# Kernel optimization log

Measured on AMD Instinct MI355X. Metric: run time of the kernel, lower is better.

The kernel has to match this reference:

```python
import jax, jax.numpy as jnp
import numpy as np

USER_NUM = 500000
ITEM_NUM = 100000
D = 256        # embedding_size
MEM = 32       # memory_size
ATT = 256      # attention_size
B = 4096       # batch
NF = 64        # friends per user (padded with index == USER_NUM)


def _u(k, shape):
    return jax.random.uniform(k, shape, dtype=jnp.float32, minval=-0.1, maxval=0.1)


def setup_inputs() -> dict:
    key = jax.random.key(0)
    ks = jax.random.split(key, 12)
    return {
        "input_u": jax.random.randint(ks[0], (B,), 0, USER_NUM + 1),
        "input_i": jax.random.randint(ks[1], (B,), 0, ITEM_NUM),
        "input_uf": jax.random.randint(ks[2], (B, NF), 0, USER_NUM + 1),
        "uidW": _u(ks[3], (USER_NUM + 1, D)),
        "iidW": _u(ks[4], (ITEM_NUM, D)),
        "i_bias": jnp.zeros((ITEM_NUM,), jnp.float32),
        "Key": _u(ks[5], (D, MEM)),
        "Mem": jnp.ones((MEM, D), jnp.float32),
        "WA": _u(ks[6], (D, ATT)),
        "BA": jnp.zeros((ATT,), jnp.float32),
        "U_omega": _u(ks[7], (ATT, 1)),
        "att_exp1": jax.random.normal(ks[8], (2 * D, 2), jnp.float32) * 0.05,
    }


def _l2norm(x, axis):
    # torch F.normalize(p=2): x / max(||x||, eps)
    n = jnp.sqrt(jnp.sum(x * x, axis=axis, keepdims=True))
    return x / jnp.maximum(n, 1e-12)


def reference(input_u, input_i, input_uf, uidW, iidW, i_bias, Key, Mem, WA, BA, U_omega, att_exp1):
    uid = uidW[input_u]                        # [B, D]
    iid = iidW[input_i]                        # [B, D]
    i_b = i_bias[input_i]                      # [B]
    fe = uidW[input_uf]                        # [B, F, D]
    frien_num = (input_uf != USER_NUM).astype(jnp.float32)  # [B, F] valid mask
    fe = frien_num[:, :, None] * fe

    uid_n = _l2norm(uid, axis=1)
    fe_n = _l2norm(fe, axis=2)
    cross = uid_n[:, None, :] * fe_n           # [B, F, D]

    att_key = jnp.einsum('bfd,dm->bfm', cross, Key)          # [B, F, M]
    att_mem = jax.nn.softmax(att_key, axis=0)                # NOTE: softmax over BATCH dim (faithful)
    att_mem = frien_num[:, :, None] * att_mem

    f1 = jnp.einsum('bfm,md->bfd', att_mem, Mem)             # [B, F, D]
    f2 = f1 * fe                                             # [B, F, D]

    h = jax.nn.relu(jnp.einsum('bfd,da->bfa', f2, WA) + BA)  # [B, F, A]
    j = jnp.exp(jnp.einsum('bfa,ao->bfo', h, U_omega))       # [B, F, 1]
    j = frien_num[:, :, None] * j
    w = j / (jnp.sum(j, axis=1, keepdims=True) + 1e-8)       # [B, F, 1]
    friend = jnp.sum(w * f2, axis=1)                         # [B, D]
    # dropout(p=dp) in eval mode -> identity

    user = uid + friend
    att1 = jax.nn.softmax(jnp.concatenate([uid, user], axis=1) @ att_exp1, axis=1)  # [B, 2]
    user_f = uid * att1[:, 0:1] + user * att1[:, 1:2]
    score = jnp.sum(user_f * iid, axis=1) + i_b              # [B]
    return score
```

## Files before the change

### kernel.cpp

```cpp
#include <hip/hip_runtime.h>

#define USER_NUM 500000
#define BATCH 4096
#define NF 64
#define DIM 256
#define MEMN 32
#define ATTN 256

typedef short bf16x8 __attribute__((ext_vector_type(8)));
typedef float f32x4 __attribute__((ext_vector_type(4)));

__device__ __forceinline__ unsigned short f2bf(float f) {
    unsigned u = __float_as_uint(f);
    u += 0x7FFFu + ((u >> 16) & 1u);
    return (unsigned short)(u >> 16);
}
__device__ __forceinline__ float bf2f(unsigned short s) {
    return __uint_as_float(((unsigned)s) << 16);
}
__device__ __forceinline__ bf16x8 as_frag(uint4 v) {
    return __builtin_bit_cast(bf16x8, v);
}

__device__ __forceinline__ float block_reduce_sum(float v, float* scr) {
#pragma unroll
    for (int o = 32; o; o >>= 1) v += __shfl_xor(v, o, 64);
    __syncthreads();
    if ((threadIdx.x & 63) == 0) scr[threadIdx.x >> 6] = v;
    __syncthreads();
    return scr[0] + scr[1] + scr[2] + scr[3];
}

#define WS_AK    0u
#define WS_FE    33554432u
#define WS_KEYT  167772160u
#define WS_MEMT  167788544u
#define WS_WATT  167804928u
#define WS_PART  167936000u
#define WS_SSUM  168001536u

__global__ __launch_bounds__(256) void kprep(const float* __restrict__ Key,
                                             const float* __restrict__ Mem,
                                             const float* __restrict__ WA,
                                             unsigned short* __restrict__ keyT,
                                             unsigned short* __restrict__ memT,
                                             unsigned short* __restrict__ watt) {
    int gid = blockIdx.x * 256 + threadIdx.x;
    if (gid < 8192) {
        int m = gid >> 8, d = gid & 255;
        keyT[gid] = f2bf(Key[d * 32 + m]);
    } else if (gid < 16384) {
        int e = gid - 8192, d = e >> 5, m = e & 31;
        memT[e] = f2bf(Mem[m * 256 + d]);
    } else {
        int e = gid - 16384;
        int kt = e >> 13, r = e & 8191, a = r >> 5, kk = r & 31;
        watt[e] = f2bf(WA[(kt * 32 + kk) * 256 + a]);
    }
}

__global__ __launch_bounds__(256, 4) void katt(const int* __restrict__ input_u,
                                               const int* __restrict__ input_uf,
                                               const float* __restrict__ uidW,
                                               const unsigned short* __restrict__ keyT_ws,
                                               unsigned short* __restrict__ fe_ws,
                                               float* __restrict__ ak) {
    extern __shared__ char smem[];
    float* uidn = (float*)(smem + 33792);
    float* scr  = (float*)(smem + 34816);
    int*   ufL  = (int*)(smem + 34880);
    float* mskL = (float*)(smem + 35136);
    const int b = blockIdx.x, t = threadIdx.x;
    const int w = t >> 6, l = t & 63, q = l >> 4;

    if (t < 64) {
        int uf = input_uf[b * NF + t];
        ufL[t] = uf;
        mskL[t] = (uf != USER_NUM) ? 1.0f : 0.0f;
    }
    int iu = input_u[b];
    float uv = uidW[(size_t)iu * DIM + t];
    float ss = block_reduce_sum(uv * uv, scr);
    float inv = 1.0f / fmaxf(sqrtf(ss), 1e-12f);
    uidn[t] = uv * inv;
    __syncthreads();

    float4 un4 = *(const float4*)(uidn + l * 4);
    float4 fe[16];
#pragma unroll
    for (int i = 0; i < 16; i++) {
        int idx = ufL[w * 16 + i];
        fe[i] = ((const float4*)(uidW + (size_t)idx * DIM))[l];
    }
#pragma unroll
    for (int i = 0; i < 16; i++) {
        int f = w * 16 + i;
        float mk = mskL[f];
        float x = fe[i].x * mk, y = fe[i].y * mk, z = fe[i].z * mk, ww = fe[i].w * mk;
        float s2 = x * x + y * y + z * z + ww * ww;
#pragma unroll
        for (int o = 32; o; o >>= 1) s2 += __shfl_xor(s2, o, 64);
        float rn = 1.0f / fmaxf(sqrtf(s2), 1e-12f);
        ushort4 fb;
        fb.x = f2bf(x); fb.y = f2bf(y); fb.z = f2bf(z); fb.w = f2bf(ww);
        *(ushort4*)(fe_ws + (size_t)b * 16384 + f * 256 + l * 4) = fb;
        ushort4 o4;
        o4.x = f2bf(un4.x * x * rn);
        o4.y = f2bf(un4.y * y * rn);
        o4.z = f2bf(un4.z * z * rn);
        o4.w = f2bf(un4.w * ww * rn);
        *(ushort4*)(smem + f * 528 + l * 8) = o4;
    }
    __syncthreads();

    const uint4* kp = (const uint4*)keyT_ws;
    f32x4 acc0 = {0.f, 0.f, 0.f, 0.f}, acc1 = {0.f, 0.f, 0.f, 0.f};
#pragma unroll
    for (int kt = 0; kt < 8; kt++) {
        bf16x8 aF = *(const bf16x8*)(smem + (w * 16 + (l & 15)) * 528 + kt * 64 + q * 16);
        bf16x8 b0 = as_frag(kp[(l & 15) * 32 + kt * 4 + q]);
        bf16x8 b1 = as_frag(kp[((l & 15) + 16) * 32 + kt * 4 + q]);
        acc0 = __builtin_amdgcn_mfma_f32_16x16x32_bf16(aF, b0, acc0, 0, 0, 0);
        acc1 = __builtin_amdgcn_mfma_f32_16x16x32_bf16(aF, b1, acc1, 0, 0, 0);
    }
    {
        int fbase = w * 16 + q * 4;
        int m = l & 15;
#pragma unroll
        for (int r = 0; r < 4; r++) {
            ak[((size_t)b * NF + fbase + r) * MEMN + m]      = acc0[r];
            ak[((size_t)b * NF + fbase + r) * MEMN + 16 + m] = acc1[r];
        }
    }
}

__global__ __launch_bounds__(256) void ksum1(const float* __restrict__ ak, float* __restrict__ part) {
    __shared__ float pl[256];
    int bid = blockIdx.x;
    int f = bid >> 3, c = bid & 7;
    int t = threadIdx.x, m = t & 31, g = t >> 5;
    float s = 0.f;
    size_t base = ((size_t)(c * 512 + g) * NF + f) * MEMN + m;
    for (int i = 0; i < 64; i++) {
        s += __expf(ak[base]);
        base += (size_t)8 * NF * MEMN;
    }
    pl[t] = s;
    __syncthreads();
    if (t < 32) {
        float tot = 0.f;
#pragma unroll
        for (int gg = 0; gg < 8; gg++) tot += pl[gg * 32 + t];
        part[c * 2048 + f * 32 + t] = tot;
    }
}
__global__ __launch_bounds__(256) void ksum2(const float* __restrict__ part, float* __restrict__ ssum) {
    int fm = blockIdx.x * 256 + threadIdx.x;
    float s = 0.f;
#pragma unroll
    for (int c = 0; c < 8; c++) s += part[c * 2048 + fm];
    ssum[fm] = s;
}

#define OFF_AM   33792
#define OFF_JP   38912
#define OFF_W    39936
#define OFF_MSK  40448
#define OFF_SCR  40704
__global__ __launch_bounds__(256, 3) void kmain(const int* __restrict__ input_u,
                                                const int* __restrict__ input_i,
                                                const int* __restrict__ input_uf,
                                                const float* __restrict__ uidW,
                                                const float* __restrict__ iidW,
                                                const float* __restrict__ i_bias,
                                                const float* __restrict__ BA,
                                                const float* __restrict__ U_omega,
                                                const float* __restrict__ att_exp1,
                                                const float* __restrict__ ak,
                                                const float* __restrict__ ssum_ws,
                                                const unsigned short* __restrict__ fe_ws,
                                                const unsigned short* __restrict__ memT_ws,
                                                const unsigned short* __restrict__ watt_ws,
                                                float* __restrict__ out) {
    extern __shared__ char smem[];
    float* jpL  = (float*)(smem + OFF_JP);
    float* wL   = (float*)(smem + OFF_W);
    float* mskL = (float*)(smem + OFF_MSK);
    float* scr  = (float*)(smem + OFF_SCR);
    const int b = blockIdx.x, t = threadIdx.x;
    const int w = t >> 6, l = t & 63, q = l >> 4;

    int iu = input_u[b], ii = input_i[b];
    float uidv = uidW[(size_t)iu * DIM + t];
    float iidv = iidW[(size_t)ii * DIM + t];
    float ib   = i_bias[ii];
    float ae00 = att_exp1[t * 2], ae01 = att_exp1[t * 2 + 1];
    float ae10 = att_exp1[(DIM + t) * 2], ae11 = att_exp1[(DIM + t) * 2 + 1];

    if (t < 64) {
        int uf = input_uf[b * NF + t];
        mskL[t] = (uf != USER_NUM) ? 1.0f : 0.0f;
    }
    __syncthreads();

    {
        const float4* akp = (const float4*)(ak + (size_t)b * 2048);
        const float4* sp  = (const float4*)ssum_ws;
        float4 a0 = akp[2 * t], a1 = akp[2 * t + 1];
        float4 s0 = sp[2 * t],  s1 = sp[2 * t + 1];
        float mk = mskL[t >> 2];
        float v0 = mk * __expf(a0.x) / s0.x;
        float v1 = mk * __expf(a0.y) / s0.y;
        float v2 = mk * __expf(a0.z) / s0.z;
        float v3 = mk * __expf(a0.w) / s0.w;
        float v4 = mk * __expf(a1.x) / s1.x;
        float v5 = mk * __expf(a1.y) / s1.y;
        float v6 = mk * __expf(a1.z) / s1.z;
        float v7 = mk * __expf(a1.w) / s1.w;
        uint4 pk;
        pk.x = (unsigned)f2bf(v0) | ((unsigned)f2bf(v1) << 16);
        pk.y = (unsigned)f2bf(v2) | ((unsigned)f2bf(v3) << 16);
        pk.z = (unsigned)f2bf(v4) | ((unsigned)f2bf(v5) << 16);
        pk.w = (unsigned)f2bf(v6) | ((unsigned)f2bf(v7) << 16);
        *(uint4*)(smem + OFF_AM + (t >> 2) * 80 + (t & 3) * 16) = pk;
    }
    __syncthreads();

    {
        const uint4* mp = (const uint4*)memT_ws;
        bf16x8 aF[4];
#pragma unroll
        for (int ft = 0; ft < 4; ft++)
            aF[ft] = *(const bf16x8*)(smem + OFF_AM + (ft * 16 + (l & 15)) * 80 + q * 16);
#pragma unroll
        for (int dti = 0; dti < 4; dti++) {
            int dt = 4 * w + dti;
            bf16x8 bF = as_frag(mp[(dt * 16 + (l & 15)) * 4 + q]);
            int dcol = dt * 16 + (l & 15);
#pragma unroll
            for (int ft = 0; ft < 4; ft++) {
                f32x4 acc = {0.f, 0.f, 0.f, 0.f};
                acc = __builtin_amdgcn_mfma_f32_16x16x32_bf16(aF[ft], bF, acc, 0, 0, 0);
                int fbase = ft * 16 + q * 4;
#pragma unroll
                for (int r = 0; r < 4; r++)
                    *(unsigned short*)(smem + (fbase + r) * 528 + dcol * 2) = f2bf(acc[r]);
            }
        }
    }
    __syncthreads();

    {
        ushort4 feb[16];
#pragma unroll
        for (int i = 0; i < 16; i++) {
            int f = w * 16 + i;
            feb[i] = *(const ushort4*)(fe_ws + (size_t)b * 16384 + f * 256 + l * 4);
        }
#pragma unroll
        for (int i = 0; i < 16; i++) {
            int f = w * 16 + i;
            ushort4* p = (ushort4*)(smem + f * 528 + l * 8);
            ushort4 fv = *p;
            ushort4 o4;
            o4.x = f2bf(bf2f(fv.x) * bf2f(feb[i].x));
            o4.y = f2bf(bf2f(fv.y) * bf2f(feb[i].y));
            o4.z = f2bf(bf2f(fv.z) * bf2f(feb[i].z));
            o4.w = f2bf(bf2f(fv.w) * bf2f(feb[i].w));
            *p = o4;
        }
    }
    __syncthreads();

    f32x4 acc[4][4];
    {
        f32x4 z = {0.f, 0.f, 0.f, 0.f};
#pragma unroll
        for (int ft = 0; ft < 4; ft++)
#pragma unroll
            for (int at = 0; at < 4; at++) acc[ft][at] = z;
    }
    {
        const uint4* wp = (const uint4*)watt_ws;
        for (int kt = 0; kt < 8; kt++) {
            bf16x8 aF[4], bF[4];
#pragma unroll
            for (int ft = 0; ft < 4; ft++)
                aF[ft] = *(const bf16x8*)(smem + (ft * 16 + (l & 15)) * 528 + kt * 64 + q * 16);
#pragma unroll
            for (int at = 0; at < 4; at++)
                bF[at] = as_frag(wp[kt * 1024 + (64 * w + at * 16 + (l & 15)) * 4 + q]);
#pragma unroll
            for (int ft = 0; ft < 4; ft++)
#pragma unroll
                for (int at = 0; at < 4; at++)
                    acc[ft][at] = __builtin_amdgcn_mfma_f32_16x16x32_bf16(aF[ft], bF[at], acc[ft][at], 0, 0, 0);
        }
    }
    {
        float jp[16];
#pragma unroll
        for (int i = 0; i < 16; i++) jp[i] = 0.f;
#pragma unroll
        for (int at = 0; at < 4; at++) {
            int a = 64 * w + at * 16 + (l & 15);
            float ba = BA[a], uw = U_omega[a];
#pragma unroll
            for (int ft = 0; ft < 4; ft++)
#pragma unroll
                for (int r = 0; r < 4; r++) {
                    float h = fmaxf(acc[ft][at][r] + ba, 0.f);
                    jp[ft * 4 + r] += h * uw;
                }
        }
#pragma unroll
        for (int mask = 1; mask < 16; mask <<= 1)
#pragma unroll
            for (int i = 0; i < 16; i++) jp[i] += __shfl_xor(jp[i], mask, 64);
        if ((l & 15) == 0) {
#pragma unroll
            for (int ft = 0; ft < 4; ft++)
#pragma unroll
                for (int r = 0; r < 4; r++)
                    jpL[w * 64 + ft * 16 + q * 4 + r] = jp[ft * 4 + r];
        }
    }
    __syncthreads();

    if (t < 64) {
        float logit = jpL[t] + jpL[64 + t] + jpL[128 + t] + jpL[192 + t];
        float jv = mskL[t] * __expf(logit);
        float s = jv;
#pragma unroll
        for (int o = 32; o; o >>= 1) s += __shfl_xor(s, o, 64);
        wL[t] = jv / (s + 1e-8f);
    }
    __syncthreads();

    float fr = 0.f;
#pragma unroll 8
    for (int f = 0; f < 64; f++)
        fr += wL[f] * bf2f(*(unsigned short*)(smem + f * 528 + t * 2));

    float user = uidv + fr;
    float l0 = block_reduce_sum(uidv * ae00 + user * ae10, scr);
    float l1 = block_reduce_sum(uidv * ae01 + user * ae11, scr);
    float mx = fmaxf(l0, l1);
    float e0 = __expf(l0 - mx), e1 = __expf(l1 - mx);
    float rinv = 1.0f / (e0 + e1);
    float a0w = e0 * rinv, a1w = e1 * rinv;
    float sc = block_reduce_sum((uidv * a0w + user * a1w) * iidv, scr);
    if (t == 0) out[b] = sc + ib;
}

extern "C" void kernel_launch(void* const* d_in, const int* in_sizes, int n_in,
                              void* d_out, int out_size, void* d_ws, size_t ws_size,
                              hipStream_t stream) {
    const int*   input_u  = (const int*)d_in[0];
    const int*   input_i  = (const int*)d_in[1];
    const int*   input_uf = (const int*)d_in[2];
    const float* uidW     = (const float*)d_in[3];
    const float* iidW     = (const float*)d_in[4];
    const float* i_bias   = (const float*)d_in[5];
    const float* Key      = (const float*)d_in[6];
    const float* Mem      = (const float*)d_in[7];
    const float* WA       = (const float*)d_in[8];
    const float* BA       = (const float*)d_in[9];
    const float* U_omega  = (const float*)d_in[10];
    const float* att_exp1 = (const float*)d_in[11];
    float* out = (float*)d_out;
    char* ws = (char*)d_ws;

    float*          ak   = (float*)(ws + WS_AK);
    unsigned short* fe   = (unsigned short*)(ws + WS_FE);
    unsigned short* keyT = (unsigned short*)(ws + WS_KEYT);
    unsigned short* memT = (unsigned short*)(ws + WS_MEMT);
    unsigned short* watt = (unsigned short*)(ws + WS_WATT);
    float*          part = (float*)(ws + WS_PART);
    float*          ssum = (float*)(ws + WS_SSUM);

    hipLaunchKernelGGL(kprep, dim3(320), dim3(256), 0, stream, Key, Mem, WA, keyT, memT, watt);
    hipLaunchKernelGGL(katt, dim3(BATCH), dim3(256), 35392, stream, input_u, input_uf, uidW, keyT, fe, ak);
    hipLaunchKernelGGL(ksum1, dim3(512), dim3(256), 0, stream, ak, part);
    hipLaunchKernelGGL(ksum2, dim3(8), dim3(256), 0, stream, part, ssum);
    hipLaunchKernelGGL(kmain, dim3(BATCH), dim3(256), 40768, stream, input_u, input_i, input_uf,
                       uidW, iidW, i_bias, BA, U_omega, att_exp1, ak, ssum, fe, memT, watt, out);
}
```

Measured before the change: 802.7 us.

## Store exp once in katt, store reciprocal sums, hoist loads, fuse reductions

katt now writes exp(att_key) directly, so ksum1 sums it without exp and kmain multiplies by a stored reciprocal of the column sum instead of redoing exp and a divide. The friend index gather in katt moves from shared memory to shuffles and is issued before the uid norm reduction, and kmain loads its fe fragments early and computes masks from indices, dropping a sync. Mem/WA conversion moves from kprep into ksum2, and the two logit block reductions are merged into one. Several unrelated micro changes; storing exp unnormalised risks overflow only for large logits, which the small weights make unlikely.

New measurement: 791.3 us. About the same (-1.4%).

```diff
diff --git a/kernel.cpp b/kernel.cpp
--- a/kernel.cpp
+++ b/kernel.cpp
@@ -29,6 +29,24 @@
     if ((threadIdx.x & 63) == 0) scr[threadIdx.x >> 6] = v;
     __syncthreads();
     return scr[0] + scr[1] + scr[2] + scr[3];
+}
+
+__device__ __forceinline__ float2 block_reduce_sum2(float a, float b, float* scr) {
+#pragma unroll
+    for (int o = 32; o; o >>= 1) {
+        a += __shfl_xor(a, o, 64);
+        b += __shfl_xor(b, o, 64);
+    }
+    __syncthreads();
+    if ((threadIdx.x & 63) == 0) {
+        scr[(threadIdx.x >> 6) * 2]     = a;
+        scr[(threadIdx.x >> 6) * 2 + 1] = b;
+    }
+    __syncthreads();
+    float2 r;
+    r.x = scr[0] + scr[2] + scr[4] + scr[6];
+    r.y = scr[1] + scr[3] + scr[5] + scr[7];
+    return r;
 }
 
 #define WS_AK    0u
@@ -40,23 +58,10 @@
 #define WS_SSUM  168001536u
 
 __global__ __launch_bounds__(256) void kprep(const float* __restrict__ Key,
-                                             const float* __restrict__ Mem,
-                                             const float* __restrict__ WA,
-                                             unsigned short* __restrict__ keyT,
-                                             unsigned short* __restrict__ memT,
-                                             unsigned short* __restrict__ watt) {
+                                             unsigned short* __restrict__ keyT) {
     int gid = blockIdx.x * 256 + threadIdx.x;
-    if (gid < 8192) {
-        int m = gid >> 8, d = gid & 255;
-        keyT[gid] = f2bf(Key[d * 32 + m]);
-    } else if (gid < 16384) {
-        int e = gid - 8192, d = e >> 5, m = e & 31;
-        memT[e] = f2bf(Mem[m * 256 + d]);
-    } else {
-        int e = gid - 16384;
-        int kt = e >> 13, r = e & 8191, a = r >> 5, kk = r & 31;
-        watt[e] = f2bf(WA[(kt * 32 + kk) * 256 + a]);
-    }
+    int m = gid >> 8, d = gid & 255;
+    keyT[gid] = f2bf(Key[d * 32 + m]);
 }
 
 __global__ __launch_bounds__(256, 4) void katt(const int* __restrict__ input_u,
@@ -68,34 +73,30 @@
     extern __shared__ char smem[];
     float* uidn = (float*)(smem + 33792);
     float* scr  = (float*)(smem + 34816);
-    int*   ufL  = (int*)(smem + 34880);
-    float* mskL = (float*)(smem + 35136);
     const int b = blockIdx.x, t = threadIdx.x;
     const int w = t >> 6, l = t & 63, q = l >> 4;
 
-    if (t < 64) {
-        int uf = input_uf[b * NF + t];
-        ufL[t] = uf;
-        mskL[t] = (uf != USER_NUM) ? 1.0f : 0.0f;
-    }
-    int iu = input_u[b];
+    int iu   = input_u[b];
+    int myuf = input_uf[b * NF + w * 16 + (l & 15)];
     float uv = uidW[(size_t)iu * DIM + t];
+
+    float4 fe[16];
+#pragma unroll
+    for (int i = 0; i < 16; i++) {
+        int idx = __shfl(myuf, i, 64);
+        fe[i] = ((const float4*)(uidW + (size_t)idx * DIM))[l];
+    }
+
     float ss = block_reduce_sum(uv * uv, scr);
     float inv = 1.0f / fmaxf(sqrtf(ss), 1e-12f);
     uidn[t] = uv * inv;
     __syncthreads();
 
     float4 un4 = *(const float4*)(uidn + l * 4);
-    float4 fe[16];
-#pragma unroll
-    for (int i = 0; i < 16; i++) {
-        int idx = ufL[w * 16 + i];
-        fe[i] = ((const float4*)(uidW + (size_t)idx * DIM))[l];
-    }
 #pragma unroll
     for (int i = 0; i < 16; i++) {
         int f = w * 16 + i;
-        float mk = mskL[f];
+        float mk = (__shfl(myuf, i, 64) != USER_NUM) ? 1.0f : 0.0f;
         float x = fe[i].x * mk, y = fe[i].y * mk, z = fe[i].z * mk, ww = fe[i].w * mk;
         float s2 = x * x + y * y + z * z + ww * ww;
 #pragma unroll
@@ -128,8 +129,8 @@
         int m = l & 15;
 #pragma unroll
         for (int r = 0; r < 4; r++) {
-            ak[((size_t)b * NF + fbase + r) * MEMN + m]      = acc0[r];
-            ak[((size_t)b * NF + fbase + r) * MEMN + 16 + m] = acc1[r];
+            ak[((size_t)b * NF + fbase + r) * MEMN + m]      = __expf(acc0[r]);
+            ak[((size_t)b * NF + fbase + r) * MEMN + 16 + m] = __expf(acc1[r]);
         }
     }
 }
@@ -141,8 +142,9 @@
     int t = threadIdx.x, m = t & 31, g = t >> 5;
     float s = 0.f;
     size_t base = ((size_t)(c * 512 + g) * NF + f) * MEMN + m;
+#pragma unroll 8
     for (int i = 0; i < 64; i++) {
-        s += __expf(ak[base]);
+        s += ak[base];
         base += (size_t)8 * NF * MEMN;
     }
     pl[t] = s;
@@ -154,18 +156,30 @@
         part[c * 2048 + f * 32 + t] = tot;
     }
 }
-__global__ __launch_bounds__(256) void ksum2(const float* __restrict__ part, float* __restrict__ ssum) {
+__global__ __launch_bounds__(256) void ksum2(const float* __restrict__ part,
+                                             float* __restrict__ ssum,
+                                             const float* __restrict__ Mem,
+                                             const float* __restrict__ WA,
+                                             unsigned short* __restrict__ memT,
+                                             unsigned short* __restrict__ watt) {
     int fm = blockIdx.x * 256 + threadIdx.x;
     float s = 0.f;
 #pragma unroll
     for (int c = 0; c < 8; c++) s += part[c * 2048 + fm];
-    ssum[fm] = s;
+    ssum[fm] = 1.0f / s;
+    for (int e = fm; e < 8192; e += 2048) {
+        int d = e >> 5, m = e & 31;
+        memT[e] = f2bf(Mem[m * 256 + d]);
+    }
+    for (int e = fm; e < 65536; e += 2048) {
+        int kt = e >> 13, r = e & 8191, a = r >> 5, kk = r & 31;
+        watt[e] = f2bf(WA[(kt * 32 + kk) * 256 + a]);
+    }
 }
 
 #define OFF_AM   33792
 #define OFF_JP   38912
 #define OFF_W    39936
-#define OFF_MSK  40448
 #define OFF_SCR  40704
 __global__ __launch_bounds__(256, 3) void kmain(const int* __restrict__ input_u,
                                                 const int* __restrict__ input_i,
@@ -185,7 +199,6 @@
     extern __shared__ char smem[];
     float* jpL  = (float*)(smem + OFF_JP);
     float* wL   = (float*)(smem + OFF_W);
-    float* mskL = (float*)(smem + OFF_MSK);
     float* scr  = (float*)(smem + OFF_SCR);
     const int b = blockIdx.x, t = threadIdx.x;
     const int w = t >> 6, l = t & 63, q = l >> 4;
@@ -196,27 +209,27 @@
     float ib   = i_bias[ii];
     float ae00 = att_exp1[t * 2], ae01 = att_exp1[t * 2 + 1];
     float ae10 = att_exp1[(DIM + t) * 2], ae11 = att_exp1[(DIM + t) * 2 + 1];
-
-    if (t < 64) {
-        int uf = input_uf[b * NF + t];
-        mskL[t] = (uf != USER_NUM) ? 1.0f : 0.0f;
-    }
-    __syncthreads();
-
-    {
-        const float4* akp = (const float4*)(ak + (size_t)b * 2048);
-        const float4* sp  = (const float4*)ssum_ws;
-        float4 a0 = akp[2 * t], a1 = akp[2 * t + 1];
-        float4 s0 = sp[2 * t],  s1 = sp[2 * t + 1];
-        float mk = mskL[t >> 2];
-        float v0 = mk * __expf(a0.x) / s0.x;
-        float v1 = mk * __expf(a0.y) / s0.y;
-        float v2 = mk * __expf(a0.z) / s0.z;
-        float v3 = mk * __expf(a0.w) / s0.w;
-        float v4 = mk * __expf(a1.x) / s1.x;
-        float v5 = mk * __expf(a1.y) / s1.y;
-        float v6 = mk * __expf(a1.z) / s1.z;
-        float v7 = mk * __expf(a1.w) / s1.w;
+    int uf_f = input_uf[b * NF + (t >> 2)];
+    int uf_t = input_uf[b * NF + (t & 63)];
+    const float4* akp = (const float4*)(ak + (size_t)b * 2048);
+    const float4* rp  = (const float4*)ssum_ws;
+    float4 a0 = akp[2 * t], a1 = akp[2 * t + 1];
+    float4 r0 = rp[2 * t],  r1 = rp[2 * t + 1];
+    ushort4 feb[16];
+#pragma unroll
+    for (int i = 0; i < 16; i++)
+        feb[i] = *(const ushort4*)(fe_ws + (size_t)b * 16384 + (w * 16 + i) * 256 + l * 4);
+
+    {
+        float mk = (uf_f != USER_NUM) ? 1.0f : 0.0f;
+        float v0 = mk * a0.x * r0.x;
+        float v1 = mk * a0.y * r0.y;
+        float v2 = mk * a0.z * r0.z;
+        float v3 = mk * a0.w * r0.w;
+        float v4 = mk * a1.x * r1.x;
+        float v5 = mk * a1.y * r1.y;
+        float v6 = mk * a1.z * r1.z;
+        float v7 = mk * a1.w * r1.w;
         uint4 pk;
         pk.x = (unsigned)f2bf(v0) | ((unsigned)f2bf(v1) << 16);
         pk.y = (unsigned)f2bf(v2) | ((unsigned)f2bf(v3) << 16);
@@ -251,12 +264,6 @@
     __syncthreads();
 
     {
-        ushort4 feb[16];
-#pragma unroll
-        for (int i = 0; i < 16; i++) {
-            int f = w * 16 + i;
-            feb[i] = *(const ushort4*)(fe_ws + (size_t)b * 16384 + f * 256 + l * 4);
-        }
 #pragma unroll
         for (int i = 0; i < 16; i++) {
             int f = w * 16 + i;
@@ -329,7 +336,7 @@
 
     if (t < 64) {
         float logit = jpL[t] + jpL[64 + t] + jpL[128 + t] + jpL[192 + t];
-        float jv = mskL[t] * __expf(logit);
+        float jv = ((uf_t != USER_NUM) ? 1.0f : 0.0f) * __expf(logit);
         float s = jv;
 #pragma unroll
         for (int o = 32; o; o >>= 1) s += __shfl_xor(s, o, 64);
@@ -343,10 +350,9 @@
         fr += wL[f] * bf2f(*(unsigned short*)(smem + f * 528 + t * 2));
 
     float user = uidv + fr;
-    float l0 = block_reduce_sum(uidv * ae00 + user * ae10, scr);
-    float l1 = block_reduce_sum(uidv * ae01 + user * ae11, scr);
-    float mx = fmaxf(l0, l1);
-    float e0 = __expf(l0 - mx), e1 = __expf(l1 - mx);
+    float2 ll = block_reduce_sum2(uidv * ae00 + user * ae10, uidv * ae01 + user * ae11, scr);
+    float mx = fmaxf(ll.x, ll.y);
+    float e0 = __expf(ll.x - mx), e1 = __expf(ll.y - mx);
     float rinv = 1.0f / (e0 + e1);
     float a0w = e0 * rinv, a1w = e1 * rinv;
     float sc = block_reduce_sum((uidv * a0w + user * a1w) * iidv, scr);
@@ -379,10 +385,10 @@
     float*          part = (float*)(ws + WS_PART);
     float*          ssum = (float*)(ws + WS_SSUM);
 
-    hipLaunchKernelGGL(kprep, dim3(320), dim3(256), 0, stream, Key, Mem, WA, keyT, memT, watt);
-    hipLaunchKernelGGL(katt, dim3(BATCH), dim3(256), 35392, stream, input_u, input_uf, uidW, keyT, fe, ak);
+    hipLaunchKernelGGL(kprep, dim3(32), dim3(256), 0, stream, Key, keyT);
+    hipLaunchKernelGGL(katt, dim3(BATCH), dim3(256), 34880, stream, input_u, input_uf, uidW, keyT, fe, ak);
     hipLaunchKernelGGL(ksum1, dim3(512), dim3(256), 0, stream, ak, part);
-    hipLaunchKernelGGL(ksum2, dim3(8), dim3(256), 0, stream, part, ssum);
+    hipLaunchKernelGGL(ksum2, dim3(8), dim3(256), 0, stream, part, ssum, Mem, WA, memT, watt);
     hipLaunchKernelGGL(kmain, dim3(BATCH), dim3(256), 40768, stream, input_u, input_i, input_uf,
                        uidW, iidW, i_bias, BA, U_omega, att_exp1, ak, ssum, fe, memT, watt, out);
 }
```
